# Kernel optimization log

Hardware: AMD Instinct MI355X
Metric: run time of the kernel (lower is better)

## Reference

```python
import jax, jax.numpy as jnp
import numpy as np


def _get_pixel_value(img, x, y, z):
    # img: (B, D, H, W, C); x/y/z: int32 (B, Do, Ho, Wo)
    B = img.shape[0]
    b = jnp.arange(B, dtype=jnp.int32)[:, None, None, None]
    return img[b, z, y, x]  # (B, Do, Ho, Wo, C)


def _trilinear_sampler(img, xs, ys, zs):
    D, H, W = img.shape[1], img.shape[2], img.shape[3]
    max_x, max_y, max_z = W - 1, H - 1, D - 1
    # NOTE: original scales by (max-1), i.e. (dim-2) -- kept faithfully.
    xs = 0.5 * (xs + 1.0) * jnp.float32(max_x - 1)
    ys = 0.5 * (ys + 1.0) * jnp.float32(max_y - 1)
    zs = 0.5 * (zs + 1.0) * jnp.float32(max_z - 1)
    x0 = jnp.floor(xs).astype(jnp.int32); x1 = x0 + 1
    y0 = jnp.floor(ys).astype(jnp.int32); y1 = y0 + 1
    z0 = jnp.floor(zs).astype(jnp.int32); z1 = z0 + 1
    x0 = jnp.clip(x0, 0, max_x); x1 = jnp.clip(x1, 0, max_x)
    y0 = jnp.clip(y0, 0, max_y); y1 = jnp.clip(y1, 0, max_y)
    z0 = jnp.clip(z0, 0, max_z); z1 = jnp.clip(z1, 0, max_z)
    Ia = _get_pixel_value(img, x0, y0, z0)
    Ib = _get_pixel_value(img, x0, y1, z0)
    Ic = _get_pixel_value(img, x1, y0, z0)
    Id = _get_pixel_value(img, x1, y1, z0)
    Ie = _get_pixel_value(img, x0, y0, z1)
    If = _get_pixel_value(img, x0, y1, z1)
    Ig = _get_pixel_value(img, x1, y0, z1)
    Ih = _get_pixel_value(img, x1, y1, z1)
    x0f = x0.astype(jnp.float32); x1f = x1.astype(jnp.float32)
    y0f = y0.astype(jnp.float32); y1f = y1.astype(jnp.float32)
    z0f = z0.astype(jnp.float32); z1f = z1.astype(jnp.float32)
    wa = ((x1f - xs) * (y1f - ys) * (z1f - zs))[..., None]
    wb = ((x1f - xs) * (ys - y0f) * (z1f - zs))[..., None]
    wc = ((xs - x0f) * (y1f - ys) * (z1f - zs))[..., None]
    wd = ((xs - x0f) * (ys - y0f) * (z1f - zs))[..., None]
    we = ((x1f - xs) * (y1f - ys) * (zs - z0f))[..., None]
    wf = ((x1f - xs) * (ys - y0f) * (zs - z0f))[..., None]
    wg = ((xs - x0f) * (y1f - ys) * (zs - z0f))[..., None]
    wh = ((xs - x0f) * (ys - y0f) * (zs - z0f))[..., None]
    return (wa * Ia + wb * Ib + wc * Ic + wd * Id
            + we * Ie + wf * If + wg * Ig + wh * Ih)


def _affine_grid(depth, height, width, theta):
    d = jnp.linspace(-1.0, 1.0, depth, dtype=jnp.float32)
    h = jnp.linspace(-1.0, 1.0, height, dtype=jnp.float32)
    w = jnp.linspace(-1.0, 1.0, width, dtype=jnp.float32)
    # tf.meshgrid(h, d, w) (indexing='xy') -> outputs of shape (D, H, W):
    # x_t varies along H, z_t along D, y_t along W.
    z_t, x_t, y_t = jnp.meshgrid(d, h, w, indexing='ij')
    ones = jnp.ones_like(x_t)
    grid = jnp.stack([x_t.ravel(), y_t.ravel(), z_t.ravel(), ones.ravel()], axis=0)  # (4, N)
    batch_grids = jnp.einsum('bij,jn->bin', theta, grid)  # (B, 3, N)
    return batch_grids.reshape(theta.shape[0], 3, depth, height, width)


def reference(x, hw_d, hw_h, hw_w):
    B = x.shape[0]
    theta = jnp.tile(jnp.asarray([[[1, 0, 0, 0], [0, 1, 0, 0], [0, 0, 1, 0]]],
                                 dtype=jnp.float32), (B, 1, 1))
    gridout = _affine_grid(int(hw_d), int(hw_h), int(hw_w), theta)
    y_s = gridout[:, 0]
    x_s = gridout[:, 1]
    z_s = gridout[:, 2]
    return _trilinear_sampler(x, x_s, y_s, z_s)


def setup_inputs() -> dict:
    key = jax.random.key(0)
    x = jax.random.normal(key, (4, 64, 64, 64, 32), dtype=jnp.float32)
    return {"x": x, "hw_d": 64, "hw_h": 64, "hw_w": 64}
```

## Files before the change

### kernel.cpp

```cpp
#include <hip/hip_runtime.h>


#define BD 4
#define DD 64
#define HH 64
#define WW 64
#define CC 32
#define C4 (CC / 4)

__global__ __launch_bounds__(256) void trilerp_kernel(
    const float4* __restrict__ in, float4* __restrict__ out) {
    int t = blockIdx.x * blockDim.x + threadIdx.x;

    int cq  = t & (C4 - 1);
    int vox = t >> 3;
    int k = vox & 63;
    int j = (vox >> 6) & 63;
    int i = (vox >> 12) & 63;
    int b = vox >> 18;

    const float s = 62.0f / 63.0f;
    float xs = (float)k * s;
    float ys = (float)j * s;
    float zs = (float)i * s;

    int x0 = (int)xs;
    int y0 = (int)ys;
    int z0 = (int)zs;
    float fx = xs - (float)x0;
    float fy = ys - (float)y0;
    float fz = zs - (float)z0;
    int x1 = min(x0 + 1, WW - 1);
    int y1 = min(y0 + 1, HH - 1);
    int z1 = min(z0 + 1, DD - 1);

    int bb  = b << 21;
    int z0o = bb + (z0 << 15);
    int z1o = bb + (z1 << 15);
    int y0o = y0 << 9;
    int y1o = y1 << 9;
    int x0o = (x0 << 3) + cq;
    int x1o = (x1 << 3) + cq;

    float4 v000 = in[z0o + y0o + x0o];
    float4 v010 = in[z0o + y1o + x0o];
    float4 v001 = in[z0o + y0o + x1o];
    float4 v011 = in[z0o + y1o + x1o];
    float4 v100 = in[z1o + y0o + x0o];
    float4 v110 = in[z1o + y1o + x0o];
    float4 v101 = in[z1o + y0o + x1o];
    float4 v111 = in[z1o + y1o + x1o];

    float gx = 1.0f - fx, gy = 1.0f - fy, gz = 1.0f - fz;
    float wa = gx * gy * gz;
    float wb = gx * fy * gz;
    float wc = fx * gy * gz;
    float wd = fx * fy * gz;
    float we = gx * gy * fz;
    float wf = gx * fy * fz;
    float wg = fx * gy * fz;
    float wh = fx * fy * fz;

    float4 r;
    r.x = fmaf(v000.x, wa, fmaf(v010.x, wb, fmaf(v001.x, wc, fmaf(v011.x, wd,
          fmaf(v100.x, we, fmaf(v110.x, wf, fmaf(v101.x, wg, v111.x * wh)))))));
    r.y = fmaf(v000.y, wa, fmaf(v010.y, wb, fmaf(v001.y, wc, fmaf(v011.y, wd,
          fmaf(v100.y, we, fmaf(v110.y, wf, fmaf(v101.y, wg, v111.y * wh)))))));
    r.z = fmaf(v000.z, wa, fmaf(v010.z, wb, fmaf(v001.z, wc, fmaf(v011.z, wd,
          fmaf(v100.z, we, fmaf(v110.z, wf, fmaf(v101.z, wg, v111.z * wh)))))));
    r.w = fmaf(v000.w, wa, fmaf(v010.w, wb, fmaf(v001.w, wc, fmaf(v011.w, wd,
          fmaf(v100.w, we, fmaf(v110.w, wf, fmaf(v101.w, wg, v111.w * wh)))))));

    out[t] = r;
}

extern "C" void kernel_launch(void* const* d_in, const int* in_sizes, int n_in,
                              void* d_out, int out_size, void* d_ws, size_t ws_size,
                              hipStream_t stream) {
    const float4* in = (const float4*)d_in[0];
    float4* out = (float4*)d_out;

    const int total = BD * DD * HH * WW * C4;
    const int block = 256;
    const int grid = total / block;

    trilerp_kernel<<<grid, block, 0, stream>>>(in, out);
}
```

Before: 239.5 us.

## Compute 2x2x2 output voxels per thread with separable lerp and shared neighbors

Each thread now produces a 2x2x2 block of output voxels. Their source neighborhoods overlap in a 3x3x3 input stencil, so the thread loads 27 float4 values instead of 64 and interpolates separably along x, y and z. The kernel also remaps block IDs to spread blocks across XCDs and writes output with nontemporal stores. The exchange is higher register pressure and fewer threads. The code also assumes the fixed index pattern floor(i*62/63) lies in {2p-1, 2p}, which holds only for this shape.

```diff
diff --git a/kernel.cpp b/kernel.cpp
--- a/kernel.cpp
+++ b/kernel.cpp
@@ -1,77 +1,110 @@
 #include <hip/hip_runtime.h>
 
 
-#define BD 4
-#define DD 64
-#define HH 64
-#define WW 64
-#define CC 32
-#define C4 (CC / 4)
+#define C4 8
+
+typedef float f4raw __attribute__((ext_vector_type(4)));
+
+__device__ __forceinline__ void nt_store(float4 v, float4* p) {
+    __builtin_nontemporal_store(*reinterpret_cast<f4raw*>(&v),
+                                reinterpret_cast<f4raw*>(p));
+}
+
+__device__ __forceinline__ float4 f4lerp(float4 a, float wa, float4 b, float wb) {
+    float4 r;
+    r.x = fmaf(a.x, wa, b.x * wb);
+    r.y = fmaf(a.y, wa, b.y * wb);
+    r.z = fmaf(a.z, wa, b.z * wb);
+    r.w = fmaf(a.w, wa, b.w * wb);
+    return r;
+}
+
+__device__ __forceinline__ float4 f4scale(float4 a, float w) {
+    float4 r;
+    r.x = a.x * w; r.y = a.y * w; r.z = a.z * w; r.w = a.w * w;
+    return r;
+}
+
+__device__ __forceinline__ void f4acc(float4& c, float4 a, float w) {
+    c.x = fmaf(a.x, w, c.x);
+    c.y = fmaf(a.y, w, c.y);
+    c.z = fmaf(a.z, w, c.z);
+    c.w = fmaf(a.w, w, c.w);
+}
 
 __global__ __launch_bounds__(256) void trilerp_kernel(
     const float4* __restrict__ in, float4* __restrict__ out) {
-    int t = blockIdx.x * blockDim.x + threadIdx.x;
+    int bid  = (int)blockIdx.x;
+    int sbid = (bid & 7) * ((int)gridDim.x >> 3) + (bid >> 3);
+    int t    = sbid * 256 + (int)threadIdx.x;
 
-    int cq  = t & (C4 - 1);
-    int vox = t >> 3;
-    int k = vox & 63;
-    int j = (vox >> 6) & 63;
-    int i = (vox >> 12) & 63;
-    int b = vox >> 18;
+    int cq = t & 7;
+    int kp = (t >> 3) & 31;
+    int j2 = (t >> 8) & 31;
+    int i2 = (t >> 13) & 31;
+    int b  = t >> 18;
+
+    int x1 = kp << 1, x2 = x1 + 1, x0 = (x1 > 0) ? x1 - 1 : 0;
+    int y1 = j2 << 1, y2 = y1 + 1, y0 = (y1 > 0) ? y1 - 1 : 0;
+    int z1 = i2 << 1, z2 = z1 + 1, z0 = (z1 > 0) ? z1 - 1 : 0;
 
     const float s = 62.0f / 63.0f;
-    float xs = (float)k * s;
-    float ys = (float)j * s;
-    float zs = (float)i * s;
-
-    int x0 = (int)xs;
-    int y0 = (int)ys;
-    int z0 = (int)zs;
-    float fx = xs - (float)x0;
-    float fy = ys - (float)y0;
-    float fz = zs - (float)z0;
-    int x1 = min(x0 + 1, WW - 1);
-    int y1 = min(y0 + 1, HH - 1);
-    int z1 = min(z0 + 1, DD - 1);
+    float tx0 = (float)x1 * s; float fx0 = tx0 - (float)(int)tx0; float gx0 = 1.0f - fx0;
+    float tx1 = (float)x2 * s; float fx1 = tx1 - (float)(int)tx1; float gx1 = 1.0f - fx1;
+    float ty0 = (float)y1 * s; float fy0 = ty0 - (float)(int)ty0; float gy0 = 1.0f - fy0;
+    float ty1 = (float)y2 * s; float fy1 = ty1 - (float)(int)ty1; float gy1 = 1.0f - fy1;
+    float tz0 = (float)z1 * s; float fz0 = tz0 - (float)(int)tz0; float gz0 = 1.0f - fz0;
+    float tz1 = (float)z2 * s; float fz1 = tz1 - (float)(int)tz1; float gz1 = 1.0f - fz1;
 
     int bb  = b << 21;
-    int z0o = bb + (z0 << 15);
-    int z1o = bb + (z1 << 15);
-    int y0o = y0 << 9;
-    int y1o = y1 << 9;
-    int x0o = (x0 << 3) + cq;
-    int x1o = (x1 << 3) + cq;
+    int ry0 = y0 << 9, ry1 = y1 << 9, ry2 = y2 << 9;
+    int xo0 = (x0 << 3) + cq, xo1 = (x1 << 3) + cq, xo2 = (x2 << 3) + cq;
 
-    float4 v000 = in[z0o + y0o + x0o];
-    float4 v010 = in[z0o + y1o + x0o];
-    float4 v001 = in[z0o + y0o + x1o];
-    float4 v011 = in[z0o + y1o + x1o];
-    float4 v100 = in[z1o + y0o + x0o];
-    float4 v110 = in[z1o + y1o + x0o];
-    float4 v101 = in[z1o + y0o + x1o];
-    float4 v111 = in[z1o + y1o + x1o];
+    float4 by00, by01, by10, by11;
 
-    float gx = 1.0f - fx, gy = 1.0f - fy, gz = 1.0f - fz;
-    float wa = gx * gy * gz;
-    float wb = gx * fy * gz;
-    float wc = fx * gy * gz;
-    float wd = fx * fy * gz;
-    float we = gx * gy * fz;
-    float wf = gx * fy * fz;
-    float wg = fx * gy * fz;
-    float wh = fx * fy * fz;
+#define PLANE(ZP) do {                                                         \
+        const float4* __restrict__ P = in + (bb + ((ZP) << 15));               \
+        float4 e0a = P[ry0 + xo0], e0b = P[ry0 + xo1], e0c = P[ry0 + xo2];     \
+        float4 e1a = P[ry1 + xo0], e1b = P[ry1 + xo1], e1c = P[ry1 + xo2];     \
+        float4 e2a = P[ry2 + xo0], e2b = P[ry2 + xo1], e2c = P[ry2 + xo2];     \
+        float4 bx0l = f4lerp(e0a, gx0, e0b, fx0);                              \
+        float4 bx0r = f4lerp(e0b, gx1, e0c, fx1);                              \
+        float4 bx1l = f4lerp(e1a, gx0, e1b, fx0);                              \
+        float4 bx1r = f4lerp(e1b, gx1, e1c, fx1);                              \
+        float4 bx2l = f4lerp(e2a, gx0, e2b, fx0);                              \
+        float4 bx2r = f4lerp(e2b, gx1, e2c, fx1);                              \
+        by00 = f4lerp(bx0l, gy0, bx1l, fy0);                                   \
+        by01 = f4lerp(bx0r, gy0, bx1r, fy0);                                   \
+        by10 = f4lerp(bx1l, gy1, bx2l, fy1);                                   \
+        by11 = f4lerp(bx1r, gy1, bx2r, fy1);                                   \
+    } while (0)
 
-    float4 r;
-    r.x = fmaf(v000.x, wa, fmaf(v010.x, wb, fmaf(v001.x, wc, fmaf(v011.x, wd,
-          fmaf(v100.x, we, fmaf(v110.x, wf, fmaf(v101.x, wg, v111.x * wh)))))));
-    r.y = fmaf(v000.y, wa, fmaf(v010.y, wb, fmaf(v001.y, wc, fmaf(v011.y, wd,
-          fmaf(v100.y, we, fmaf(v110.y, wf, fmaf(v101.y, wg, v111.y * wh)))))));
-    r.z = fmaf(v000.z, wa, fmaf(v010.z, wb, fmaf(v001.z, wc, fmaf(v011.z, wd,
-          fmaf(v100.z, we, fmaf(v110.z, wf, fmaf(v101.z, wg, v111.z * wh)))))));
-    r.w = fmaf(v000.w, wa, fmaf(v010.w, wb, fmaf(v001.w, wc, fmaf(v011.w, wd,
-          fmaf(v100.w, we, fmaf(v110.w, wf, fmaf(v101.w, wg, v111.w * wh)))))));
+    PLANE(z0);
+    float4 o000 = f4scale(by00, gz0), o001 = f4scale(by01, gz0);
+    float4 o010 = f4scale(by10, gz0), o011 = f4scale(by11, gz0);
 
-    out[t] = r;
+    PLANE(z1);
+    f4acc(o000, by00, fz0); f4acc(o001, by01, fz0);
+    f4acc(o010, by10, fz0); f4acc(o011, by11, fz0);
+    float4 o100 = f4scale(by00, gz1), o101 = f4scale(by01, gz1);
+    float4 o110 = f4scale(by10, gz1), o111 = f4scale(by11, gz1);
+
+    PLANE(z2);
+    f4acc(o100, by00, fz1); f4acc(o101, by01, fz1);
+    f4acc(o110, by10, fz1); f4acc(o111, by11, fz1);
+
+#undef PLANE
+
+    int base = bb + (y1 << 9) + (x1 << 3) + cq;
+    int zb1  = z1 << 15, zb2 = z2 << 15;
+    nt_store(o000, &out[base + zb1]);
+    nt_store(o001, &out[base + zb1 + 8]);
+    nt_store(o010, &out[base + zb1 + 512]);
+    nt_store(o011, &out[base + zb1 + 520]);
+    nt_store(o100, &out[base + zb2]);
+    nt_store(o101, &out[base + zb2 + 8]);
+    nt_store(o110, &out[base + zb2 + 512]);
+    nt_store(o111, &out[base + zb2 + 520]);
 }
 
 extern "C" void kernel_launch(void* const* d_in, const int* in_sizes, int n_in,
@@ -80,9 +113,9 @@
     const float4* in = (const float4*)d_in[0];
     float4* out = (float4*)d_out;
 
-    const int total = BD * DD * HH * WW * C4;
+    const int total = 4 * 32 * 32 * 32 * C4;
     const int block = 256;
-    const int grid = total / block;
+    const int grid  = total / block;
 
     trilerp_kernel<<<grid, block, 0, stream>>>(in, out);
 }
```

After: 246.3 us. +2.8%, slower.
